# Kernel tuning notes

Hardware: AMD Instinct MI355X
Metric: run time of the kernel (lower is better)

## Reference

```python
import jax, jax.numpy as jnp
import numpy as np

D_MODEL = 512
D_STATE = 16
D_CONV = 2
DT_RANK = D_MODEL // 16  # mamba default dt_rank = ceil(d_model/16)
D_INNER = D_MODEL        # expand = 1
B, L = 4, 2048
LN_EPS = 1e-5


def setup_inputs() -> dict:
    key = jax.random.key(0)
    ks = jax.random.split(key, 16)
    s = 0.02
    inp = {
        "x_signal": jax.random.normal(ks[0], (B, L, D_MODEL), jnp.float32),
        "x_stats": jax.random.normal(ks[1], (B, 1, D_MODEL), jnp.float32),
        # GatedCrossAttention params (torch Linear weight layout: (out, in))
        "gW1": jax.random.normal(ks[2], (D_MODEL, 2 * D_MODEL), jnp.float32) * s,
        "gb1": jnp.zeros((D_MODEL,), jnp.float32),
        "gW2": jax.random.normal(ks[3], (1, D_MODEL), jnp.float32) * s,
        "gb2": jnp.zeros((1,), jnp.float32),
        "ln_g": jnp.ones((D_MODEL,), jnp.float32),
        "ln_b": jnp.zeros((D_MODEL,), jnp.float32),
        # Mamba params
        "in_proj_W": jax.random.normal(ks[4], (2 * D_INNER, D_MODEL), jnp.float32) * s,
        "conv_w": jax.random.normal(ks[5], (D_INNER, D_CONV), jnp.float32) * s,
        "conv_b": jnp.zeros((D_INNER,), jnp.float32),
        "x_proj_W": jax.random.normal(ks[6], (DT_RANK + 2 * D_STATE, D_INNER), jnp.float32) * s,
        "dt_proj_W": jax.random.normal(ks[7], (D_INNER, DT_RANK), jnp.float32) * s,
        "dt_proj_b": jnp.full((D_INNER,), -4.6, jnp.float32),  # softplus ~ 0.01
        "A_log": jnp.log(jnp.broadcast_to(jnp.arange(1, D_STATE + 1, dtype=jnp.float32), (D_INNER, D_STATE))),
        "Dp": jnp.ones((D_INNER,), jnp.float32),
        "out_proj_W": jax.random.normal(ks[8], (D_MODEL, D_INNER), jnp.float32) * s,
    }
    return inp


def _silu(x):
    return x * jax.nn.sigmoid(x)


def _forward(x_signal, x_stats, gW1, gb1, gW2, gb2, ln_g, ln_b,
             in_proj_W, conv_w, conv_b, x_proj_W, dt_proj_W, dt_proj_b,
             A_log, Dp, out_proj_W):
    # ---- GatedCrossAttention ----
    xs = jnp.broadcast_to(x_stats, x_signal.shape)           # (B,L,D)
    gi = jnp.concatenate([x_signal, xs], axis=-1)            # (B,L,2D)
    h = jax.nn.relu(gi @ gW1.T + gb1)
    gate = jax.nn.sigmoid(h @ gW2.T + gb2)                   # (B,L,1)
    x = x_signal + gate * xs
    mu = jnp.mean(x, -1, keepdims=True)
    var = jnp.var(x, -1, keepdims=True)
    x = (x - mu) * jax.lax.rsqrt(var + LN_EPS) * ln_g + ln_b  # (B,L,D)

    # ---- Mamba (d_state=16, d_conv=2, expand=1) ----
    xz = x @ in_proj_W.T                                     # (B,L,2*Din)
    u, z = jnp.split(xz, 2, axis=-1)
    # causal depthwise conv1d, kernel size 2
    up = jnp.pad(u, ((0, 0), (D_CONV - 1, 0), (0, 0)))
    uc = conv_b + sum(conv_w[:, k] * up[:, k:k + u.shape[1]] for k in range(D_CONV))
    u = _silu(uc)                                            # (B,L,Din)

    xdbc = u @ x_proj_W.T                                    # (B,L,dt_rank+2N)
    dt = xdbc[..., :DT_RANK]
    Bm = xdbc[..., DT_RANK:DT_RANK + D_STATE]                # (B,L,N)
    Cm = xdbc[..., DT_RANK + D_STATE:]                       # (B,L,N)
    delta = jax.nn.softplus(dt @ dt_proj_W.T + dt_proj_b)    # (B,L,Din)

    A = -jnp.exp(A_log)                                      # (Din,N)
    dA = jnp.exp(delta[..., None] * A)                       # (B,L,Din,N)
    dBu = delta[..., None] * Bm[:, :, None, :] * u[..., None]

    def step(hst, inps):
        dA_t, dBu_t, C_t = inps
        hst = dA_t * hst + dBu_t                             # (B,Din,N)
        y_t = jnp.einsum('bdn,bn->bd', hst, C_t)
        return hst, y_t

    h0 = jnp.zeros((u.shape[0], D_INNER, D_STATE), u.dtype)
    xs_scan = (jnp.swapaxes(dA, 0, 1), jnp.swapaxes(dBu, 0, 1), jnp.swapaxes(Cm, 0, 1))
    _, ys = jax.lax.scan(step, h0, xs_scan)                  # (L,B,Din)
    y = jnp.swapaxes(ys, 0, 1) + Dp * u
    y = y * _silu(z)
    out = y @ out_proj_W.T                                   # (B,L,D)
    # dropout is identity in eval mode
    return out


def reference(x_signal, x_stats, gW1, gb1, gW2, gb2, ln_g, ln_b,
              in_proj_W, conv_w, conv_b, x_proj_W, dt_proj_W, dt_proj_b,
              A_log, Dp, out_proj_W):
    return _forward(x_signal, x_stats, gW1, gb1, gW2, gb2, ln_g, ln_b,
                    in_proj_W, conv_w, conv_b, x_proj_W, dt_proj_W, dt_proj_b,
                    A_log, Dp, out_proj_W)
```

## Files before the change

kernel.cpp:

```cpp
#include <hip/hip_runtime.h>
#include <hip/hip_bf16.h>
#include <math.h>

#define D_MODEL 512
#define D_STATE 16
#define DT_RANK 32
#define D_INNER 512
#define BB 4
#define LL 2048
#define MROWS (BB * LL)
#define LN_EPS 1e-5f
#define CHUNK 32
#define NCH (LL / CHUNK)
#define LOG2E 1.44269504f
#define LN2 0.69314718f

typedef __bf16 bf16x8 __attribute__((ext_vector_type(8)));
typedef float f32x4 __attribute__((ext_vector_type(4)));

__device__ __forceinline__ ushort f2bf(float x) {
  uint u = __float_as_uint(x);
  u = (u + 0x7fffu + ((u >> 16) & 1u)) >> 16;
  return (ushort)u;
}
__device__ __forceinline__ float bf2f(ushort h) {
  return __uint_as_float(((uint)h) << 16);
}
__device__ __forceinline__ void split2(float x, ushort& hi, ushort& lo) {
  hi = f2bf(x);
  lo = f2bf(x - bf2f(hi));
}

__device__ __forceinline__ void gload_lds16(const void* g, void* l) {
  __builtin_amdgcn_global_load_lds(
      (const __attribute__((address_space(1))) uint32_t*)g,
      (__attribute__((address_space(3))) uint32_t*)l, 16, 0, 0);
}

template <int EPI>
__global__ __launch_bounds__(256) void gemm_mfma(const ushort* __restrict__ Ahi,
                                                 const ushort* __restrict__ Alo,
                                                 const ushort* __restrict__ Bhi,
                                                 const ushort* __restrict__ Blo,
                                                 float* __restrict__ C, int ldc, int K,
                                                 int nx, const float* __restrict__ e0,
                                                 const float* __restrict__ g2,
                                                 float* __restrict__ sdot) {
  __shared__ ushort sA[2][2][128][32];
  __shared__ ushort sB[2][2][64][32];

  const int tid = threadIdx.x;
  const int lane = tid & 63;
  const int wid = tid >> 6;

  const int nwg = gridDim.x;
  const int q = nwg >> 3;
  const int t = (blockIdx.x & 7) * q + (blockIdx.x >> 3);
  const int bx = t % nx;
  const int by = t / nx;
  const int m0 = by * 128;
  const int n0 = bx * 64;

  const int srow = tid >> 2;
  const int koff = (((tid & 3) ^ ((tid >> 3) & 3)) << 3);
  const ushort* Ah_p = Ahi + (size_t)(m0 + srow) * K + koff;
  const ushort* Al_p = Alo + (size_t)(m0 + srow) * K + koff;
  const ushort* Bh_p = Bhi + (size_t)(n0 + srow) * K + koff;
  const ushort* Bl_p = Blo + (size_t)(n0 + srow) * K + koff;
  const size_t rstep = (size_t)64 * K;
  const int wb = wid * 16;

  const int wr = wid >> 1, wc = wid & 1;
  const int fr = lane & 15;
  const int rcs = (((lane >> 4) ^ ((fr >> 1) & 3)) << 3);

  f32x4 acc[4][2] = {};

  auto STAGE = [&](int bq, int kk) {
    gload_lds16(Ah_p + kk,         &sA[bq][0][wb][0]);
    gload_lds16(Ah_p + kk + rstep, &sA[bq][0][64 + wb][0]);
    gload_lds16(Al_p + kk,         &sA[bq][1][wb][0]);
    gload_lds16(Al_p + kk + rstep, &sA[bq][1][64 + wb][0]);
    gload_lds16(Bh_p + kk,         &sB[bq][0][wb][0]);
    gload_lds16(Bl_p + kk,         &sB[bq][1][wb][0]);
  };

  int cur = 0;
  STAGE(0, 0);
  __syncthreads();

  for (int k0 = 0; k0 < K; k0 += 32) {
    if (k0 + 32 < K) STAGE(cur ^ 1, k0 + 32);
    bf16x8 ah[4], al[4], bh[2], bl[2];
#pragma unroll
    for (int m = 0; m < 4; ++m) {
      const int ar = wr * 64 + m * 16 + fr;
      ah[m] = *(const bf16x8*)&sA[cur][0][ar][rcs];
      al[m] = *(const bf16x8*)&sA[cur][1][ar][rcs];
    }
#pragma unroll
    for (int n = 0; n < 2; ++n) {
      const int br = wc * 32 + n * 16 + fr;
      bh[n] = *(const bf16x8*)&sB[cur][0][br][rcs];
      bl[n] = *(const bf16x8*)&sB[cur][1][br][rcs];
    }
#pragma unroll
    for (int m = 0; m < 4; ++m)
#pragma unroll
      for (int n = 0; n < 2; ++n) {
        acc[m][n] = __builtin_amdgcn_mfma_f32_16x16x32_bf16(ah[m], bh[n],
                                                            acc[m][n], 0, 0, 0);
        acc[m][n] = __builtin_amdgcn_mfma_f32_16x16x32_bf16(ah[m], bl[n],
                                                            acc[m][n], 0, 0, 0);
        acc[m][n] = __builtin_amdgcn_mfma_f32_16x16x32_bf16(al[m], bh[n],
                                                            acc[m][n], 0, 0, 0);
      }
    __syncthreads();
    cur ^= 1;
  }

  const int rbase = (lane >> 4) * 4;
  if (EPI == 1) {
    const int c0 = n0 + wc * 32 + fr;
    const int c1c = n0 + wc * 32 + 16 + fr;
    const float g2a = g2[c0];
    const float g2b = g2[c1c];
#pragma unroll
    for (int m = 0; m < 4; ++m) {
#pragma unroll
      for (int r = 0; r < 4; ++r) {
        const int row = m0 + wr * 64 + m * 16 + rbase + r;
        const int bofs = (row >> 11) * D_MODEL;
        const float v0 = fmaxf(acc[m][0][r] + e0[bofs + c0], 0.f);
        const float v1 = fmaxf(acc[m][1][r] + e0[bofs + c1c], 0.f);
        float val = fmaf(v0, g2a, v1 * g2b);
        val += __shfl_xor(val, 1);
        val += __shfl_xor(val, 2);
        val += __shfl_xor(val, 4);
        val += __shfl_xor(val, 8);
        if (fr == 0) atomicAdd(&sdot[row], val);
      }
    }
  } else {
#pragma unroll
    for (int m = 0; m < 4; ++m) {
      const int row0 = m0 + wr * 64 + m * 16 + rbase;
#pragma unroll
      for (int n = 0; n < 2; ++n) {
        const int col = n0 + wc * 32 + n * 16 + fr;
#pragma unroll
        for (int r = 0; r < 4; ++r)
          C[(size_t)(row0 + r) * ldc + col] = acc[m][n][r];
      }
    }
  }
}

#define SA_(bq, hl, row) smem[bq][hl][row]
#define SB_(bq, hl, row) smem[bq][hl][128 + (row)]
__global__ __launch_bounds__(256) void xproj_fused(const ushort* __restrict__ Ahi,
                                                   const ushort* __restrict__ Alo,
                                                   const ushort* __restrict__ Wchi,
                                                   const ushort* __restrict__ Wclo,
                                                   const ushort* __restrict__ Wbhi,
                                                   const ushort* __restrict__ Wblo,
                                                   float* __restrict__ DELTA,
                                                   const float* __restrict__ dtb,
                                                   float* __restrict__ BC) {
  __shared__ ushort smem[2][2][192][32];
  const int K = 512;
  const int tid = threadIdx.x;
  const int lane = tid & 63;
  const int wid = tid >> 6;
  const int fr = lane & 15;
  const int rcs = (((lane >> 4) ^ ((fr >> 1) & 3)) << 3);
  const int rbase = (lane >> 4) * 4;
  const int wr = wid >> 1, wc = wid & 1;

  if (blockIdx.x < 512) {
    const int bid = blockIdx.x;
    const int q = 512 >> 3;
    const int t = (bid & 7) * q + (bid >> 3);
    const int bx = t % 8;
    const int by = t / 8;
    const int m0 = by * 128;
    const int n0 = bx * 64;

    const int srow = tid >> 2;
    const int koff = (((tid & 3) ^ ((tid >> 3) & 3)) << 3);
    const ushort* Ah_p = Ahi + (size_t)(m0 + srow) * K + koff;
    const ushort* Al_p = Alo + (size_t)(m0 + srow) * K + koff;
    const ushort* Bh_p = Wchi + (size_t)(n0 + srow) * K + koff;
    const ushort* Bl_p = Wclo + (size_t)(n0 + srow) * K + koff;
    const size_t rstep = (size_t)64 * K;
    const int wb = wid * 16;

    f32x4 acc[4][2] = {};

    auto STAGE = [&](int bq, int kk) {
      gload_lds16(Ah_p + kk,         &SA_(bq, 0, wb)[0]);
      gload_lds16(Ah_p + kk + rstep, &SA_(bq, 0, 64 + wb)[0]);
      gload_lds16(Al_p + kk,         &SA_(bq, 1, wb)[0]);
      gload_lds16(Al_p + kk + rstep, &SA_(bq, 1, 64 + wb)[0]);
      gload_lds16(Bh_p + kk,         &SB_(bq, 0, wb)[0]);
      gload_lds16(Bl_p + kk,         &SB_(bq, 1, wb)[0]);
    };

    int cur = 0;
    STAGE(0, 0);
    __syncthreads();

    for (int k0 = 0; k0 < K; k0 += 32) {
      if (k0 + 32 < K) STAGE(cur ^ 1, k0 + 32);
      bf16x8 ah[4], al[4], bh[2], bl[2];
#pragma unroll
      for (int m = 0; m < 4; ++m) {
        const int ar = wr * 64 + m * 16 + fr;
        ah[m] = *(const bf16x8*)&SA_(cur, 0, ar)[rcs];
        al[m] = *(const bf16x8*)&SA_(cur, 1, ar)[rcs];
      }
#pragma unroll
      for (int n = 0; n < 2; ++n) {
        const int br = wc * 32 + n * 16 + fr;
        bh[n] = *(const bf16x8*)&SB_(cur, 0, br)[rcs];
        bl[n] = *(const bf16x8*)&SB_(cur, 1, br)[rcs];
      }
#pragma unroll
      for (int m = 0; m < 4; ++m)
#pragma unroll
        for (int n = 0; n < 2; ++n) {
          acc[m][n] = __builtin_amdgcn_mfma_f32_16x16x32_bf16(ah[m], bh[n],
                                                              acc[m][n], 0, 0, 0);
          acc[m][n] = __builtin_amdgcn_mfma_f32_16x16x32_bf16(ah[m], bl[n],
                                                              acc[m][n], 0, 0, 0);
          acc[m][n] = __builtin_amdgcn_mfma_f32_16x16x32_bf16(al[m], bh[n],
                                                              acc[m][n], 0, 0, 0);
        }
      __syncthreads();
      cur ^= 1;
    }

#pragma unroll
    for (int m = 0; m < 4; ++m) {
      const int row0 = m0 + wr * 64 + m * 16 + rbase;
#pragma unroll
      for (int n = 0; n < 2; ++n) {
        const int col = n0 + wc * 32 + n * 16 + fr;
#pragma unroll
        for (int r = 0; r < 4; ++r) {
          const float x = acc[m][n][r] + dtb[col];
          const float e = __builtin_amdgcn_exp2f(-fabsf(x) * LOG2E);
          DELTA[(size_t)(row0 + r) * 512 + col] =
              fmaxf(x, 0.f) + __log2f(1.f + e) * LN2;
        }
      }
    }
  } else {
    const int m0 = (blockIdx.x - 512) * 64;
    const int srow = lane >> 2;
    const int koff = (((lane & 3) ^ ((lane >> 3) & 3)) << 3);
    const ushort* Ah_p = Ahi + (size_t)(m0 + wid * 16 + srow) * K + koff;
    const ushort* Al_p = Alo + (size_t)(m0 + wid * 16 + srow) * K + koff;
    const ushort* B_p = ((wid < 2) ? Wbhi : Wblo) +
                        (size_t)((wid & 1) * 16 + srow) * K + koff;

    f32x4 acc[2] = {};

    auto STAGE = [&](int bq, int kk) {
      gload_lds16(Ah_p + kk, &SA_(bq, 0, wid * 16)[0]);
      gload_lds16(Al_p + kk, &SA_(bq, 1, wid * 16)[0]);
      gload_lds16(B_p + kk, &SB_(bq, wid >> 1, (wid & 1) * 16)[0]);
    };

    int cur = 0;
    STAGE(0, 0);
    __syncthreads();

    for (int k0 = 0; k0 < K; k0 += 32) {
      if (k0 + 32 < K) STAGE(cur ^ 1, k0 + 32);
      bf16x8 ah[2], al[2], bh, bl;
#pragma unroll
      for (int m = 0; m < 2; ++m) {
        const int ar = wr * 32 + m * 16 + fr;
        ah[m] = *(const bf16x8*)&SA_(cur, 0, ar)[rcs];
        al[m] = *(const bf16x8*)&SA_(cur, 1, ar)[rcs];
      }
      const int br = wc * 16 + fr;
      bh = *(const bf16x8*)&SB_(cur, 0, br)[rcs];
      bl = *(const bf16x8*)&SB_(cur, 1, br)[rcs];
#pragma unroll
      for (int m = 0; m < 2; ++m) {
        acc[m] = __builtin_amdgcn_mfma_f32_16x16x32_bf16(ah[m], bh, acc[m], 0, 0, 0);
        acc[m] = __builtin_amdgcn_mfma_f32_16x16x32_bf16(ah[m], bl, acc[m], 0, 0, 0);
        acc[m] = __builtin_amdgcn_mfma_f32_16x16x32_bf16(al[m], bh, acc[m], 0, 0, 0);
      }
      __syncthreads();
      cur ^= 1;
    }

    const int col = wc * 16 + fr;
#pragma unroll
    for (int m = 0; m < 2; ++m) {
      const int row0 = m0 + wr * 32 + m * 16 + rbase;
#pragma unroll
      for (int r = 0; r < 4; ++r)
        BC[(size_t)(row0 + r) * 32 + col] = acc[m][r];
    }
  }
}

__global__ __launch_bounds__(256) void prep_all(const float* __restrict__ x,
                                                const float* __restrict__ gW1,
                                                const float* __restrict__ ipW,
                                                const float* __restrict__ opW,
                                                const float* __restrict__ xW,
                                                const float* __restrict__ dtW,
                                                const float* __restrict__ xstats,
                                                const float* __restrict__ gb1,
                                                ushort* __restrict__ XShi,
                                                ushort* __restrict__ XSlo,
                                                ushort* __restrict__ Whi,
                                                ushort* __restrict__ Wlo,
                                                float* __restrict__ c1,
                                                float* __restrict__ sgate) {
  const int blk = blockIdx.x;
  const int tid = threadIdx.x;
  if (blk < 4096) {
    const int i = (blk * 256 + tid) * 4;
    float4 v = *(const float4*)(x + i);
    ushort h0, l0, h1, l1, h2, l2, h3, l3;
    split2(v.x, h0, l0); split2(v.y, h1, l1);
    split2(v.z, h2, l2); split2(v.w, h3, l3);
    ushort4 hv = {h0, h1, h2, h3}, lv = {l0, l1, l2, l3};
    *(ushort4*)(XShi + i) = hv;
    *(ushort4*)(XSlo + i) = lv;
    return;
  }
  if (blk < 4096 + 1296) {
    const int sub = tid >> 7;
    const int tt = tid & 127;
    const int r = (blk - 4096) * 2 + sub;
    const int j = r - 2048;
    __shared__ float sdt[2][32];
    if (tt < 32 && j >= 0 && j < 512) sdt[sub][tt] = dtW[j * 32 + tt];
    __syncthreads();
    float v[4] = {0.f, 0.f, 0.f, 0.f};
    if (r < 2048) {
      const float* src = (r < 512)    ? gW1 + (size_t)r * 1024
                         : (r < 1536) ? ipW + (size_t)(r - 512) * 512
                                      : opW + (size_t)(r - 1536) * 512;
      const float4 xv = *(const float4*)(src + tt * 4);
      v[0] = xv.x; v[1] = xv.y; v[2] = xv.z; v[3] = xv.w;
    } else if (j < 512) {
      const int k = tt * 4;
#pragma unroll 8
      for (int rr = 0; rr < 32; ++rr) {
        const float w = sdt[sub][rr];
        const float4 xv = *(const float4*)(xW + rr * 512 + k);
        v[0] = fmaf(w, xv.x, v[0]);
        v[1] = fmaf(w, xv.y, v[1]);
        v[2] = fmaf(w, xv.z, v[2]);
        v[3] = fmaf(w, xv.w, v[3]);
      }
    } else {
      const float4 xv = *(const float4*)(xW + (size_t)(32 + j - 512) * 512 + tt * 4);
      v[0] = xv.x; v[1] = xv.y; v[2] = xv.z; v[3] = xv.w;
    }
    ushort h[4], l[4];
#pragma unroll
    for (int c = 0; c < 4; ++c) split2(v[c], h[c], l[c]);
    const size_t off = (size_t)r * 512 + tt * 4;
    ushort4 hv = {h[0], h[1], h[2], h[3]}, lv = {l[0], l[1], l[2], l[3]};
    *(ushort4*)(Whi + off) = hv;
    *(ushort4*)(Wlo + off) = lv;
    return;
  }
  if (blk < 4096 + 1296 + 8) {
    const int c = blk - (4096 + 1296);
    const int b = c >> 1;
    const int j = ((c & 1) << 8) + tid;
    float acc = gb1[j];
    const float* xs = xstats + b * D_MODEL;
    const float* w = gW1 + (size_t)j * (2 * D_MODEL) + D_MODEL;
    for (int k = 0; k < D_MODEL; k += 4) {
      acc = fmaf(xs[k], w[k], acc);
      acc = fmaf(xs[k + 1], w[k + 1], acc);
      acc = fmaf(xs[k + 2], w[k + 2], acc);
      acc = fmaf(xs[k + 3], w[k + 3], acc);
    }
    c1[b * D_MODEL + j] = acc;
    return;
  }
  const int i = ((blk - (4096 + 1296 + 8)) * 256 + tid) * 4;
  float4 z = {0.f, 0.f, 0.f, 0.f};
  *(float4*)(sgate + i) = z;
}

__device__ __forceinline__ float block_sum(float v, float* sm) {
#pragma unroll
  for (int m = 32; m; m >>= 1) v += __shfl_xor(v, m);
  const int lane = threadIdx.x & 63, w = threadIdx.x >> 6;
  __syncthreads();
  if (!lane) sm[w] = v;
  __syncthreads();
  return sm[0] + sm[1] + sm[2] + sm[3];
}

__global__ __launch_bounds__(256) void gate_ln_kernel(const float* __restrict__ sdot,
                                                      const float* __restrict__ xsig,
                                                      const float* __restrict__ xstats,
                                                      const float* __restrict__ gb2,
                                                      const float* __restrict__ ln_g,
                                                      const float* __restrict__ ln_b,
                                                      ushort* __restrict__ XNhi,
                                                      ushort* __restrict__ XNlo) {
  __shared__ float red[4];
  const int row = blockIdx.x;
  const int b = row >> 11;
  const int tid = threadIdx.x;
  const size_t rb = (size_t)row * D_MODEL;

  const float gate = 1.f / (1.f + expf(-(sdot[row] + gb2[0])));

  float xr[2];
#pragma unroll
  for (int ii = 0; ii < 2; ++ii) {
    const int j = tid + ii * 256;
    xr[ii] = xsig[rb + j] + gate * xstats[b * D_MODEL + j];
  }
  float sv = xr[0] + xr[1];
  const float mu = block_sum(sv, red) * (1.f / D_MODEL);
  float s2 = (xr[0] - mu) * (xr[0] - mu) + (xr[1] - mu) * (xr[1] - mu);
  const float var = block_sum(s2, red) * (1.f / D_MODEL);
  const float inv = rsqrtf(var + LN_EPS);
#pragma unroll
  for (int ii = 0; ii < 2; ++ii) {
    const int j = tid + ii * 256;
    const float v = (xr[ii] - mu) * inv * ln_g[j] + ln_b[j];
    ushort h, l;
    split2(v, h, l);
    XNhi[rb + j] = h;
    XNlo[rb + j] = l;
  }
}

__global__ __launch_bounds__(256) void conv_silu_kernel(const float* __restrict__ XZ,
                                                        const float* __restrict__ conv_w,
                                                        const float* __restrict__ conv_b,
                                                        ushort* __restrict__ Uhi,
                                                        ushort* __restrict__ Ulo) {
  const int base = blockIdx.x * 16;
  const int j = threadIdx.x * 2;
  const float w0a = conv_w[j * 2 + 0], w1a = conv_w[j * 2 + 1];
  const float w0b = conv_w[j * 2 + 2], w1b = conv_w[j * 2 + 3];
  const float ba = conv_b[j], bb = conv_b[j + 1];
  float2 prev;
  if ((base & (LL - 1)) == 0) {
    prev.x = 0.f; prev.y = 0.f;
  } else {
    prev = *(const float2*)(XZ + (size_t)(base - 1) * (2 * D_INNER) + j);
  }
#pragma unroll 4
  for (int t = 0; t < 16; ++t) {
    const size_t r = base + t;
    const float2 cur = *(const float2*)(XZ + r * (2 * D_INNER) + j);
    float va = ba + w0a * prev.x + w1a * cur.x;
    float vb = bb + w0b * prev.y + w1b * cur.y;
    va = va / (1.f + __builtin_amdgcn_exp2f(-va * LOG2E));
    vb = vb / (1.f + __builtin_amdgcn_exp2f(-vb * LOG2E));
    ushort ha, la, hb, lb;
    split2(va, ha, la);
    split2(vb, hb, lb);
    ushort2 hv = {ha, hb}, lv = {la, lb};
    *(ushort2*)(Uhi + r * D_INNER + j) = hv;
    *(ushort2*)(Ulo + r * D_INNER + j) = lv;
    prev = cur;
  }
}

__global__ __launch_bounds__(256) void scan_part1(const float* __restrict__ DELTA,
                                                  const ushort* __restrict__ Uhi,
                                                  const ushort* __restrict__ Ulo,
                                                  const float* __restrict__ BC,
                                                  const float* __restrict__ A_log,
                                                  float* __restrict__ SLOC,
                                                  float* __restrict__ DSUM) {
  __shared__ __align__(16) float sBC[CHUNK][32];
  const int tid = threadIdx.x;
  const int bid = blockIdx.x;
  const int d = ((bid & 1) << 8) + tid;
  const int c = (bid >> 1) & (NCH - 1);
  const int b = bid >> 7;
  const size_t base = (size_t)b * LL + (size_t)c * CHUNK;

  {
    const int row = tid >> 3, col = (tid & 7) << 2;
    *(float4*)&sBC[row][col] = *(const float4*)(BC + (base + row) * 32 + col);
  }
  float A2[16];
#pragma unroll
  for (int n = 0; n < 16; ++n) A2[n] = -expf(A_log[d * 16 + n]) * LOG2E;
  __syncthreads();

  float S[16];
#pragma unroll
  for (int n = 0; n < 16; ++n) S[n] = 0.f;
  float dsum = 0.f;

#pragma unroll 2
  for (int t = 0; t < CHUNK; ++t) {
    const size_t r = base + t;
    const float delta = DELTA[r * D_INNER + d];
    const float u = bf2f(Uhi[r * D_INNER + d]) + bf2f(Ulo[r * D_INNER + d]);
    dsum += delta;
    const float du = delta * u;
    float Bv[16];
#pragma unroll
    for (int i = 0; i < 4; ++i)
      *(float4*)&Bv[i * 4] = *(const float4*)&sBC[t][i * 4];
#pragma unroll
    for (int n = 0; n < 16; ++n) {
      const float dA = __builtin_amdgcn_exp2f(delta * A2[n]);
      S[n] = fmaf(dA, S[n], du * Bv[n]);
    }
  }
  const size_t ci = ((size_t)b * NCH + c) * D_INNER + d;
#pragma unroll
  for (int i = 0; i < 4; ++i)
    *(float4*)(SLOC + ci * 16 + i * 4) = *(const float4*)&S[i * 4];
  DSUM[ci] = dsum;
}

__global__ __launch_bounds__(256) void scan_combine(const float* __restrict__ SLOC,
                                                    const float* __restrict__ DSUM,
                                                    const float* __restrict__ A_log,
                                                    float* __restrict__ HINIT) {
  const int idx = blockIdx.x * 256 + threadIdx.x;
  const int b = idx >> 13;
  const int d = (idx >> 4) & (D_INNER - 1);
  const int n = idx & 15;
  const float A2 = -expf(A_log[d * D_STATE + n]) * LOG2E;
  float h = 0.f;
#pragma unroll 4
  for (int c = 0; c < NCH; ++c) {
    const size_t ci = ((size_t)b * NCH + c) * D_INNER + d;
    HINIT[ci * 16 + n] = h;
    const float a = __builtin_amdgcn_exp2f(A2 * DSUM[ci]);
    h = fmaf(a, h, SLOC[ci * 16 + n]);
  }
}

__global__ __launch_bounds__(256) void scan_part3(const float* __restrict__ DELTA,
                                                  const ushort* __restrict__ Uhi,
                                                  const ushort* __restrict__ Ulo,
                                                  const float* __restrict__ BC,
                                                  const float* __restrict__ XZ,
                                                  const float* __restrict__ A_log,
                                                  const float* __restrict__ Dp,
                                                  const float* __restrict__ HINIT,
                                                  ushort* __restrict__ Yhi,
                                                  ushort* __restrict__ Ylo) {
  __shared__ __align__(16) float sBC[CHUNK][32];
  const int tid = threadIdx.x;
  const int bid = blockIdx.x;
  const int d = ((bid & 1) << 8) + tid;
  const int c = (bid >> 1) & (NCH - 1);
  const int b = bid >> 7;
  const size_t base = (size_t)b * LL + (size_t)c * CHUNK;

  {
    const int row = tid >> 3, col = (tid & 7) << 2;
    *(float4*)&sBC[row][col] = *(const float4*)(BC + (base + row) * 32 + col);
  }
  float A2[16];
#pragma unroll
  for (int n = 0; n < 16; ++n) A2[n] = -expf(A_log[d * 16 + n]) * LOG2E;
  const float Dpd = Dp[d];

  const size_t ci = ((size_t)b * NCH + c) * D_INNER + d;
  float h[16];
#pragma unroll
  for (int i = 0; i < 4; ++i)
    *(float4*)&h[i * 4] = *(const float4*)(HINIT + ci * 16 + i * 4);
  __syncthreads();

#pragma unroll 2
  for (int t = 0; t < CHUNK; ++t) {
    const size_t r = base + t;
    const float delta = DELTA[r * D_INNER + d];
    const float u = bf2f(Uhi[r * D_INNER + d]) + bf2f(Ulo[r * D_INNER + d]);
    const float z = XZ[r * (2 * D_INNER) + D_INNER + d];
    const float du = delta * u;
    float BCv[32];
#pragma unroll
    for (int i = 0; i < 8; ++i)
      *(float4*)&BCv[i * 4] = *(const float4*)&sBC[t][i * 4];
    float y = 0.f;
#pragma unroll
    for (int n = 0; n < 16; ++n) {
      const float dA = __builtin_amdgcn_exp2f(delta * A2[n]);
      h[n] = fmaf(dA, h[n], du * BCv[n]);
      y = fmaf(h[n], BCv[16 + n], y);
    }
    const float sz = z / (1.f + __builtin_amdgcn_exp2f(-z * LOG2E));
    const float o = (y + Dpd * u) * sz;
    ushort hh, ll;
    split2(o, hh, ll);
    Yhi[r * D_INNER + d] = hh;
    Ylo[r * D_INNER + d] = ll;
  }
}

extern "C" void kernel_launch(void* const* d_in, const int* in_sizes, int n_in,
                              void* d_out, int out_size, void* d_ws, size_t ws_size,
                              hipStream_t stream) {
  const float* x_signal = (const float*)d_in[0];
  const float* x_stats  = (const float*)d_in[1];
  const float* gW1      = (const float*)d_in[2];
  const float* gb1      = (const float*)d_in[3];
  const float* gW2      = (const float*)d_in[4];
  const float* gb2      = (const float*)d_in[5];
  const float* ln_g     = (const float*)d_in[6];
  const float* ln_b     = (const float*)d_in[7];
  const float* in_proj_W = (const float*)d_in[8];
  const float* conv_w   = (const float*)d_in[9];
  const float* conv_b   = (const float*)d_in[10];
  const float* x_proj_W = (const float*)d_in[11];
  const float* dt_proj_W = (const float*)d_in[12];
  const float* dt_proj_b = (const float*)d_in[13];
  const float* A_log    = (const float*)d_in[14];
  const float* Dp       = (const float*)d_in[15];
  const float* out_proj_W = (const float*)d_in[16];
  float* out = (float*)d_out;

  float* ws = (float*)d_ws;
  const size_t NE = (size_t)MROWS * D_MODEL;
  float* H    = ws;
  float* XNf  = H + NE;
  float* XZ   = XNf + NE;
  float* UHL  = XZ + 2 * NE;
  float* BC   = UHL + NE;
  float* C1   = BC + (size_t)MROWS * 32;
  float* SGATE = C1 + BB * D_MODEL;
  float* SLOC = SGATE + MROWS;
  float* DSUM = SLOC + (size_t)BB * NCH * D_INNER * D_STATE;
  float* HINIT = DSUM + (size_t)BB * NCH * D_INNER;
  float* WSP  = HINIT + (size_t)BB * NCH * D_INNER * D_STATE;

  ushort* XNhi = (ushort*)XNf;
  ushort* XNlo = XNhi + NE;
  ushort* XShi = (ushort*)XZ;
  ushort* XSlo = XShi + NE;
  ushort* Yhi  = (ushort*)H;
  ushort* Ylo  = Yhi + NE;
  ushort* Uhi  = (ushort*)UHL;
  ushort* Ulo  = Uhi + NE;
  ushort* Whi  = (ushort*)WSP;
  ushort* Wlo  = Whi + (size_t)2592 * 512;
  float* DELTA = XNf;

  prep_all<<<dim3(4096 + 1296 + 8 + 8), dim3(256), 0, stream>>>(
      x_signal, gW1, in_proj_W, out_proj_W, x_proj_W, dt_proj_W, x_stats, gb1,
      XShi, XSlo, Whi, Wlo, C1, SGATE);

  gemm_mfma<1><<<dim3(8 * 64), dim3(256), 0, stream>>>(
      XShi, XSlo, Whi, Wlo, nullptr, 0, D_MODEL, 8, C1, gW2, SGATE);

  gate_ln_kernel<<<dim3(MROWS), dim3(256), 0, stream>>>(SGATE, x_signal, x_stats,
                                                        gb2, ln_g, ln_b, XNhi, XNlo);

  gemm_mfma<0><<<dim3(16 * 64), dim3(256), 0, stream>>>(
      XNhi, XNlo, Whi + (size_t)512 * 512, Wlo + (size_t)512 * 512, XZ, 2 * D_INNER,
      D_MODEL, 16, nullptr, nullptr, nullptr);

  conv_silu_kernel<<<dim3(MROWS / 16), dim3(256), 0, stream>>>(XZ, conv_w, conv_b,
                                                               Uhi, Ulo);

  xproj_fused<<<dim3(640), dim3(256), 0, stream>>>(
      Uhi, Ulo, Whi + (size_t)2048 * 512, Wlo + (size_t)2048 * 512,
      Whi + (size_t)2560 * 512, Wlo + (size_t)2560 * 512, DELTA, dt_proj_b, BC);

  scan_part1<<<dim3(BB * NCH * 2), dim3(256), 0, stream>>>(DELTA, Uhi, Ulo, BC, A_log,
                                                           SLOC, DSUM);
  scan_combine<<<dim3(128), dim3(256), 0, stream>>>(SLOC, DSUM, A_log, HINIT);
  scan_part3<<<dim3(BB * NCH * 2), dim3(256), 0, stream>>>(DELTA, Uhi, Ulo, BC, XZ,
                                                           A_log, Dp, HINIT, Yhi, Ylo);

  gemm_mfma<0><<<dim3(8 * 64), dim3(256), 0, stream>>>(
      Yhi, Ylo, Whi + (size_t)1536 * 512, Wlo + (size_t)1536 * 512, out, D_MODEL,
      D_INNER, 8, nullptr, nullptr, nullptr);
}
```

Baseline: 183.7 us.

## Fold chunk-state combine into scan_part3, recomputing prefix per block

```diff
diff --git a/kernel.cpp b/kernel.cpp
--- a/kernel.cpp
+++ b/kernel.cpp
@@ -531,25 +531,6 @@
   DSUM[ci] = dsum;
 }
 
-__global__ __launch_bounds__(256) void scan_combine(const float* __restrict__ SLOC,
-                                                    const float* __restrict__ DSUM,
-                                                    const float* __restrict__ A_log,
-                                                    float* __restrict__ HINIT) {
-  const int idx = blockIdx.x * 256 + threadIdx.x;
-  const int b = idx >> 13;
-  const int d = (idx >> 4) & (D_INNER - 1);
-  const int n = idx & 15;
-  const float A2 = -expf(A_log[d * D_STATE + n]) * LOG2E;
-  float h = 0.f;
-#pragma unroll 4
-  for (int c = 0; c < NCH; ++c) {
-    const size_t ci = ((size_t)b * NCH + c) * D_INNER + d;
-    HINIT[ci * 16 + n] = h;
-    const float a = __builtin_amdgcn_exp2f(A2 * DSUM[ci]);
-    h = fmaf(a, h, SLOC[ci * 16 + n]);
-  }
-}
-
 __global__ __launch_bounds__(256) void scan_part3(const float* __restrict__ DELTA,
                                                   const ushort* __restrict__ Uhi,
                                                   const ushort* __restrict__ Ulo,
@@ -557,7 +538,8 @@
                                                   const float* __restrict__ XZ,
                                                   const float* __restrict__ A_log,
                                                   const float* __restrict__ Dp,
-                                                  const float* __restrict__ HINIT,
+                                                  const float* __restrict__ SLOC,
+                                                  const float* __restrict__ DSUM,
                                                   ushort* __restrict__ Yhi,
                                                   ushort* __restrict__ Ylo) {
   __shared__ __align__(16) float sBC[CHUNK][32];
@@ -576,13 +558,23 @@
 #pragma unroll
   for (int n = 0; n < 16; ++n) A2[n] = -expf(A_log[d * 16 + n]) * LOG2E;
   const float Dpd = Dp[d];
-
-  const size_t ci = ((size_t)b * NCH + c) * D_INNER + d;
+  __syncthreads();
+
   float h[16];
 #pragma unroll
-  for (int i = 0; i < 4; ++i)
-    *(float4*)&h[i * 4] = *(const float4*)(HINIT + ci * 16 + i * 4);
-  __syncthreads();
+  for (int n = 0; n < 16; ++n) h[n] = 0.f;
+  const size_t cb = (size_t)b * NCH * D_INNER + d;
+  for (int cp = 0; cp < c; ++cp) {
+    const size_t cj = cb + (size_t)cp * D_INNER;
+    const float ds = DSUM[cj];
+    float Sv[16];
+#pragma unroll
+    for (int i = 0; i < 4; ++i)
+      *(float4*)&Sv[i * 4] = *(const float4*)(SLOC + cj * 16 + i * 4);
+#pragma unroll
+    for (int n = 0; n < 16; ++n)
+      h[n] = fmaf(__builtin_amdgcn_exp2f(A2[n] * ds), h[n], Sv[n]);
+  }
 
 #pragma unroll 2
   for (int t = 0; t < CHUNK; ++t) {
@@ -644,8 +636,7 @@
   float* SGATE = C1 + BB * D_MODEL;
   float* SLOC = SGATE + MROWS;
   float* DSUM = SLOC + (size_t)BB * NCH * D_INNER * D_STATE;
-  float* HINIT = DSUM + (size_t)BB * NCH * D_INNER;
-  float* WSP  = HINIT + (size_t)BB * NCH * D_INNER * D_STATE;
+  float* WSP  = DSUM + (size_t)BB * NCH * D_INNER;
 
   ushort* XNhi = (ushort*)XNf;
   ushort* XNlo = XNhi + NE;
@@ -682,9 +673,9 @@
 
   scan_part1<<<dim3(BB * NCH * 2), dim3(256), 0, stream>>>(DELTA, Uhi, Ulo, BC, A_log,
                                                            SLOC, DSUM);
-  scan_combine<<<dim3(128), dim3(256), 0, stream>>>(SLOC, DSUM, A_log, HINIT);
   scan_part3<<<dim3(BB * NCH * 2), dim3(256), 0, stream>>>(DELTA, Uhi, Ulo, BC, XZ,
-                                                           A_log, Dp, HINIT, Yhi, Ylo);
+                                                           A_log, Dp, SLOC, DSUM,
+                                                           Yhi, Ylo);
 
   gemm_mfma<0><<<dim3(8 * 64), dim3(256), 0, stream>>>(
       Yhi, Ylo, Whi + (size_t)1536 * 512, Wlo + (size_t)1536 * 512, out, D_MODEL,
```

New measurement: 197.2 us. 7.3% more time.
